# Performance work log

Measured on AMD Instinct MI355X. Metric: run time of the kernel, lower is better.

The kernel has to match this reference:

```python
import jax, jax.numpy as jnp
import numpy as np
import itertools


def setup_inputs() -> dict:
    key = jax.random.key(0)
    k1, k2 = jax.random.split(key)
    B, D, H, W, C = 2, 160, 160, 160, 2
    vol = jax.random.normal(k1, (B, D, H, W, C), dtype=jnp.float32)
    # dense displacement field, a few voxels of motion (typical registration flow)
    trf = jax.random.normal(k2, (B, D, H, W, 3), dtype=jnp.float32) * 3.0
    return {"vol": vol, "trf": trf}


def _interp_single(vol, shift):
    """vol: [D,H,W,C], shift: [D,H,W,3] -> warped [D,H,W,C].
    Faithful to transform()+interpn(interp_method='linear', indexing='ij')."""
    volshape = vol.shape[:-1]
    nd = len(volshape)  # 3
    # mesh + shift = absolute sample locations (float)
    mesh = jnp.meshgrid(*[jnp.arange(d, dtype=jnp.float32) for d in volshape],
                        indexing='ij')
    loc = jnp.stack(mesh, axis=-1) + shift  # [D,H,W,3]

    loc0 = jnp.floor(loc)
    max_loc = jnp.array([d - 1 for d in volshape], dtype=jnp.float32)  # [3]
    loc0c = jnp.clip(loc0, 0.0, max_loc)          # clipped floor corner
    loc1c = jnp.clip(loc0c + 1.0, 0.0, max_loc)   # clipped ceil corner

    # NOTE: weights use clipped loc1 vs UNclipped loc, exactly as the TF code
    d1 = loc1c - loc        # weight paired with corner bit 0 (floor)
    d0 = 1.0 - d1           # weight paired with corner bit 1 (ceil)
    locs = (loc0c.astype(jnp.int32), loc1c.astype(jnp.int32))
    wts = (d1, d0)

    out = jnp.zeros(volshape + (vol.shape[-1],), dtype=vol.dtype)
    # 2^3 = 8 corner gathers + weighted accumulation (same as sub2ind + tf.gather)
    for c in itertools.product([0, 1], repeat=nd):
        idx = tuple(locs[c[d]][..., d] for d in range(nd))
        w = wts[c[0]][..., 0] * wts[c[1]][..., 1] * wts[c[2]][..., 2]
        out = out + w[..., None] * vol[idx]
    return out


def reference(vol, trf):
    # single_transform=False: per-sample warp (tf.map_fn over batch)
    return jax.vmap(_interp_single)(vol, trf)
```

## Files before the change

kernel.cpp:

```cpp
#include <hip/hip_runtime.h>


#define BLK 256
constexpr int Bn = 2, Dn = 160, Hn = 160, Wn = 160;
constexpr int HQ = 40;
constexpr int BLOCKS_PER_STRIP = (HQ * Wn) / BLK;

typedef float f32x2 __attribute__((ext_vector_type(2)));
typedef float f32x4 __attribute__((ext_vector_type(4), aligned(8)));

__global__ __launch_bounds__(BLK) void st_warp_kernel(
    const float* __restrict__ vol,
    const float* __restrict__ trf,
    float* __restrict__ out)
{
    const int tid = threadIdx.x;

    const int xcd = blockIdx.x & 7;
    const int j   = blockIdx.x >> 3;
    const int b   = xcd >> 2;
    const int h0  = (xcd & 3) * HQ;
    const int d   = j / BLOCKS_PER_STRIP;
    const int r   = j % BLOCKS_PER_STRIP;
    const int p   = r * BLK + tid;
    const int w   = p % Wn;
    const int h   = h0 + p / Wn;

    const int gvox = ((b * Dn + d) * Hn + h0) * Wn + p;

    __shared__ float s_trf[BLK * 3];
    const long long tbase = (long long)(gvox - tid) * 3;
    #pragma unroll
    for (int k = 0; k < 3; ++k)
        s_trf[k * BLK + tid] = __builtin_nontemporal_load(&trf[tbase + k * BLK + tid]);
    __syncthreads();
    const float sd = s_trf[tid * 3 + 0];
    const float sh = s_trf[tid * 3 + 1];
    const float sw = s_trf[tid * 3 + 2];

    float loc, c0f, c1f;

    loc = (float)d + sd;
    c0f = fminf(fmaxf(floorf(loc), 0.0f), (float)(Dn - 1));
    c1f = fminf(c0f + 1.0f, (float)(Dn - 1));
    const float wd0 = c1f - loc, wd1 = 1.0f - wd0;
    const int id0 = (int)c0f, id1 = (int)c1f;

    loc = (float)h + sh;
    c0f = fminf(fmaxf(floorf(loc), 0.0f), (float)(Hn - 1));
    c1f = fminf(c0f + 1.0f, (float)(Hn - 1));
    const float wh0 = c1f - loc, wh1 = 1.0f - wh0;
    const int ih0 = (int)c0f, ih1 = (int)c1f;

    loc = (float)w + sw;
    c0f = fminf(fmaxf(floorf(loc), 0.0f), (float)(Wn - 1));
    c1f = fminf(c0f + 1.0f, (float)(Wn - 1));
    const float ww0 = c1f - loc, ww1 = 1.0f - ww0;
    const int iw0 = (int)c0f;

    const int bo  = b * Dn;
    const int r00 = ((bo + id0) * Hn + ih0) * Wn;
    const int r01 = ((bo + id0) * Hn + ih1) * Wn;
    const int r10 = ((bo + id1) * Hn + ih0) * Wn;
    const int r11 = ((bo + id1) * Hn + ih1) * Wn;

    const bool lo = (iw0 < Wn - 1);
    const int  m  = lo ? iw0 : (Wn - 2);

    const f32x4 vA = *(const f32x4*)(vol + (((long long)(r00 + m)) << 1));
    const f32x4 vB = *(const f32x4*)(vol + (((long long)(r01 + m)) << 1));
    const f32x4 vC = *(const f32x4*)(vol + (((long long)(r10 + m)) << 1));
    const f32x4 vD = *(const f32x4*)(vol + (((long long)(r11 + m)) << 1));

    const float wA = wd0 * wh0, wB = wd0 * wh1, wC = wd1 * wh0, wD = wd1 * wh1;

    float a0x = lo ? vA.x : vA.z, a0y = lo ? vA.y : vA.w;
    float b0x = lo ? vB.x : vB.z, b0y = lo ? vB.y : vB.w;
    float c0x = lo ? vC.x : vC.z, c0y = lo ? vC.y : vC.w;
    float d0x = lo ? vD.x : vD.z, d0y = lo ? vD.y : vD.w;

    float acc0 = wA * (ww0 * a0x + ww1 * vA.z)
               + wB * (ww0 * b0x + ww1 * vB.z)
               + wC * (ww0 * c0x + ww1 * vC.z)
               + wD * (ww0 * d0x + ww1 * vD.z);
    float acc1 = wA * (ww0 * a0y + ww1 * vA.w)
               + wB * (ww0 * b0y + ww1 * vB.w)
               + wC * (ww0 * c0y + ww1 * vC.w)
               + wD * (ww0 * d0y + ww1 * vD.w);

    f32x2 res; res.x = acc0; res.y = acc1;
    __builtin_nontemporal_store(res, &((f32x2*)out)[gvox]);
}

extern "C" void kernel_launch(void* const* d_in, const int* in_sizes, int n_in,
                              void* d_out, int out_size, void* d_ws, size_t ws_size,
                              hipStream_t stream) {
    const float* vol = (const float*)d_in[0];
    const float* trf = (const float*)d_in[1];
    float* out = (float*)d_out;

    const int nvox = Bn * Dn * Hn * Wn;
    const int grid = nvox / BLK;
    st_warp_kernel<<<grid, BLK, 0, stream>>>(vol, trf, out);
}
```

Measured before the change: 335.3 us.

## Process four voxels per thread to raise gathers in flight

Each thread now handles four voxels, issuing all sixteen corner gathers before doing any of the interpolation math. This is meant to increase memory-level parallelism and reduce per-block overhead. The shared-memory staging of the displacement field is replaced by direct per-thread loads, which removes the barrier but makes the loads less coalesced. Register pressure increases, and a launch-bounds occupancy hint is added.

```diff
diff --git a/kernel.cpp b/kernel.cpp
--- a/kernel.cpp
+++ b/kernel.cpp
@@ -4,92 +4,107 @@
 #define BLK 256
 constexpr int Bn = 2, Dn = 160, Hn = 160, Wn = 160;
 constexpr int HQ = 40;
-constexpr int BLOCKS_PER_STRIP = (HQ * Wn) / BLK;
+constexpr int RSTRIP = HQ * Wn;
+constexpr int V = 4;
 
 typedef float f32x2 __attribute__((ext_vector_type(2)));
 typedef float f32x4 __attribute__((ext_vector_type(4), aligned(8)));
 
-__global__ __launch_bounds__(BLK) void st_warp_kernel(
+__global__ __launch_bounds__(BLK, 4) void st_warp_kernel(
     const float* __restrict__ vol,
     const float* __restrict__ trf,
     float* __restrict__ out)
 {
     const int tid = threadIdx.x;
-
     const int xcd = blockIdx.x & 7;
     const int j   = blockIdx.x >> 3;
     const int b   = xcd >> 2;
     const int h0  = (xcd & 3) * HQ;
-    const int d   = j / BLOCKS_PER_STRIP;
-    const int r   = j % BLOCKS_PER_STRIP;
-    const int p   = r * BLK + tid;
-    const int w   = p % Wn;
-    const int h   = h0 + p / Wn;
 
-    const int gvox = ((b * Dn + d) * Hn + h0) * Wn + p;
+    int   gvox[V];
+    float sd[V], sh[V], sw[V];
+    #pragma unroll
+    for (int k = 0; k < V; ++k) {
+        const int v   = j * (BLK * V) + k * BLK + tid;
+        const int d   = v / RSTRIP;
+        const int rem = v - d * RSTRIP;
+        const int hh  = rem / Wn;
+        const int w   = rem - hh * Wn;
+        gvox[k] = ((b * Dn + d) * Hn + (h0 + hh)) * Wn + w;
+    }
+    #pragma unroll
+    for (int k = 0; k < V; ++k) {
+        const float* tp = trf + (long long)gvox[k] * 3;
+        sd[k] = __builtin_nontemporal_load(tp + 0);
+        sh[k] = __builtin_nontemporal_load(tp + 1);
+        sw[k] = __builtin_nontemporal_load(tp + 2);
+    }
 
-    __shared__ float s_trf[BLK * 3];
-    const long long tbase = (long long)(gvox - tid) * 3;
+    f32x4 val[4 * V];
+    float wA[V], wB[V], wC[V], wD[V], w0[V], w1[V];
     #pragma unroll
-    for (int k = 0; k < 3; ++k)
-        s_trf[k * BLK + tid] = __builtin_nontemporal_load(&trf[tbase + k * BLK + tid]);
-    __syncthreads();
-    const float sd = s_trf[tid * 3 + 0];
-    const float sh = s_trf[tid * 3 + 1];
-    const float sw = s_trf[tid * 3 + 2];
+    for (int k = 0; k < V; ++k) {
+        const int v   = j * (BLK * V) + k * BLK + tid;
+        const int d   = v / RSTRIP;
+        const int rem = v - d * RSTRIP;
+        const int hh  = rem / Wn;
+        const int w   = rem - hh * Wn;
+        const int h   = h0 + hh;
 
-    float loc, c0f, c1f;
+        float loc, c0f, c1f;
 
-    loc = (float)d + sd;
-    c0f = fminf(fmaxf(floorf(loc), 0.0f), (float)(Dn - 1));
-    c1f = fminf(c0f + 1.0f, (float)(Dn - 1));
-    const float wd0 = c1f - loc, wd1 = 1.0f - wd0;
-    const int id0 = (int)c0f, id1 = (int)c1f;
+        loc = (float)d + sd[k];
+        c0f = fminf(fmaxf(floorf(loc), 0.0f), (float)(Dn - 1));
+        c1f = fminf(c0f + 1.0f, (float)(Dn - 1));
+        const float wd0 = c1f - loc, wd1 = 1.0f - wd0;
+        const int id0 = (int)c0f, id1 = (int)c1f;
 
-    loc = (float)h + sh;
-    c0f = fminf(fmaxf(floorf(loc), 0.0f), (float)(Hn - 1));
-    c1f = fminf(c0f + 1.0f, (float)(Hn - 1));
-    const float wh0 = c1f - loc, wh1 = 1.0f - wh0;
-    const int ih0 = (int)c0f, ih1 = (int)c1f;
+        loc = (float)h + sh[k];
+        c0f = fminf(fmaxf(floorf(loc), 0.0f), (float)(Hn - 1));
+        c1f = fminf(c0f + 1.0f, (float)(Hn - 1));
+        const float wh0 = c1f - loc, wh1 = 1.0f - wh0;
+        const int ih0 = (int)c0f, ih1 = (int)c1f;
 
-    loc = (float)w + sw;
-    c0f = fminf(fmaxf(floorf(loc), 0.0f), (float)(Wn - 1));
-    c1f = fminf(c0f + 1.0f, (float)(Wn - 1));
-    const float ww0 = c1f - loc, ww1 = 1.0f - ww0;
-    const int iw0 = (int)c0f;
+        loc = (float)w + sw[k];
+        c0f = fminf(fmaxf(floorf(loc), 0.0f), (float)(Wn - 1));
+        c1f = fminf(c0f + 1.0f, (float)(Wn - 1));
+        const float ww0 = c1f - loc, ww1 = 1.0f - ww0;
+        const int iw0 = (int)c0f;
 
-    const int bo  = b * Dn;
-    const int r00 = ((bo + id0) * Hn + ih0) * Wn;
-    const int r01 = ((bo + id0) * Hn + ih1) * Wn;
-    const int r10 = ((bo + id1) * Hn + ih0) * Wn;
-    const int r11 = ((bo + id1) * Hn + ih1) * Wn;
+        const bool lo = (iw0 < Wn - 1);
+        const int  m  = lo ? iw0 : (Wn - 2);
+        w0[k] = lo ? ww0 : 0.0f;
+        w1[k] = lo ? ww1 : 1.0f;
+        wA[k] = wd0 * wh0; wB[k] = wd0 * wh1;
+        wC[k] = wd1 * wh0; wD[k] = wd1 * wh1;
 
-    const bool lo = (iw0 < Wn - 1);
-    const int  m  = lo ? iw0 : (Wn - 2);
+        const int bo  = b * Dn;
+        const int r00 = ((bo + id0) * Hn + ih0) * Wn;
+        const int r01 = ((bo + id0) * Hn + ih1) * Wn;
+        const int r10 = ((bo + id1) * Hn + ih0) * Wn;
+        const int r11 = ((bo + id1) * Hn + ih1) * Wn;
 
-    const f32x4 vA = *(const f32x4*)(vol + (((long long)(r00 + m)) << 1));
-    const f32x4 vB = *(const f32x4*)(vol + (((long long)(r01 + m)) << 1));
-    const f32x4 vC = *(const f32x4*)(vol + (((long long)(r10 + m)) << 1));
-    const f32x4 vD = *(const f32x4*)(vol + (((long long)(r11 + m)) << 1));
+        val[4 * k + 0] = *(const f32x4*)(vol + (((long long)(r00 + m)) << 1));
+        val[4 * k + 1] = *(const f32x4*)(vol + (((long long)(r01 + m)) << 1));
+        val[4 * k + 2] = *(const f32x4*)(vol + (((long long)(r10 + m)) << 1));
+        val[4 * k + 3] = *(const f32x4*)(vol + (((long long)(r11 + m)) << 1));
+    }
 
-    const float wA = wd0 * wh0, wB = wd0 * wh1, wC = wd1 * wh0, wD = wd1 * wh1;
-
-    float a0x = lo ? vA.x : vA.z, a0y = lo ? vA.y : vA.w;
-    float b0x = lo ? vB.x : vB.z, b0y = lo ? vB.y : vB.w;
-    float c0x = lo ? vC.x : vC.z, c0y = lo ? vC.y : vC.w;
-    float d0x = lo ? vD.x : vD.z, d0y = lo ? vD.y : vD.w;
-
-    float acc0 = wA * (ww0 * a0x + ww1 * vA.z)
-               + wB * (ww0 * b0x + ww1 * vB.z)
-               + wC * (ww0 * c0x + ww1 * vC.z)
-               + wD * (ww0 * d0x + ww1 * vD.z);
-    float acc1 = wA * (ww0 * a0y + ww1 * vA.w)
-               + wB * (ww0 * b0y + ww1 * vB.w)
-               + wC * (ww0 * c0y + ww1 * vC.w)
-               + wD * (ww0 * d0y + ww1 * vD.w);
-
-    f32x2 res; res.x = acc0; res.y = acc1;
-    __builtin_nontemporal_store(res, &((f32x2*)out)[gvox]);
+    #pragma unroll
+    for (int k = 0; k < V; ++k) {
+        const f32x4 vA = val[4 * k + 0], vB = val[4 * k + 1];
+        const f32x4 vC = val[4 * k + 2], vD = val[4 * k + 3];
+        const float acc0 = wA[k] * (w0[k] * vA.x + w1[k] * vA.z)
+                         + wB[k] * (w0[k] * vB.x + w1[k] * vB.z)
+                         + wC[k] * (w0[k] * vC.x + w1[k] * vC.z)
+                         + wD[k] * (w0[k] * vD.x + w1[k] * vD.z);
+        const float acc1 = wA[k] * (w0[k] * vA.y + w1[k] * vA.w)
+                         + wB[k] * (w0[k] * vB.y + w1[k] * vB.w)
+                         + wC[k] * (w0[k] * vC.y + w1[k] * vC.w)
+                         + wD[k] * (w0[k] * vD.y + w1[k] * vD.w);
+        f32x2 res; res.x = acc0; res.y = acc1;
+        __builtin_nontemporal_store(res, &((f32x2*)out)[gvox[k]]);
+    }
 }
 
 extern "C" void kernel_launch(void* const* d_in, const int* in_sizes, int n_in,
@@ -100,6 +115,6 @@
     float* out = (float*)d_out;
 
     const int nvox = Bn * Dn * Hn * Wn;
-    const int grid = nvox / BLK;
+    const int grid = nvox / (BLK * V);
     st_warp_kernel<<<grid, BLK, 0, stream>>>(vol, trf, out);
 }
```

After: 312.2 us. -6.9%, faster.
